# Kernel optimization log

Hardware: AMD Instinct MI355X
Metric: run time of the kernel (lower is better)

Reference implementation:

```python
import jax, jax.numpy as jnp
import numpy as np

D_MODEL = 1024
NUM_HEADS = 16
HEAD_DIM = D_MODEL // NUM_HEADS


def setup_inputs() -> dict:
    key = jax.random.key(0)
    k1, k2, k3, k4, k5 = jax.random.split(key, 5)
    scale = 1.0 / np.sqrt(D_MODEL)
    x = jax.random.normal(k1, (2, 2048, D_MODEL), dtype=jnp.float32)
    Wqkv = jax.random.uniform(k2, (D_MODEL, 3 * D_MODEL), jnp.float32, -scale, scale)
    bqkv = jax.random.uniform(k3, (3 * D_MODEL,), jnp.float32, -scale, scale)
    Wout = jax.random.uniform(k4, (D_MODEL, D_MODEL), jnp.float32, -scale, scale)
    bout = jax.random.uniform(k5, (D_MODEL,), jnp.float32, -scale, scale)
    return {"x": x, "Wqkv": Wqkv, "bqkv": bqkv, "Wout": Wout, "bout": bout}


def reference(x, Wqkv, bqkv, Wout, bout):
    B, S, _ = x.shape
    qkv = x @ Wqkv + bqkv                                   # [B, S, 3*D]
    # reshape to [B, S, H, 3*head_dim] then to [B, H, S, 3*head_dim]
    qkv = qkv.reshape(B, S, NUM_HEADS, 3 * HEAD_DIM).transpose(0, 2, 1, 3)
    q, k, v = jnp.split(qkv, 3, axis=-1)                    # each [B, H, S, hd]
    scaled = jnp.einsum("bhqd,bhkd->bhqk", q, k) / jnp.sqrt(jnp.float32(HEAD_DIM))
    attn = jax.nn.softmax(scaled, axis=-1)                  # [B, H, S, S]
    values = jnp.einsum("bhqk,bhkd->bhqd", attn, v)         # [B, H, S, hd]
    values = values.transpose(0, 2, 1, 3).reshape(B, S, D_MODEL)
    return values @ Wout + bout
```

## Files before the change

kernel.cpp:

```cpp
#include <hip/hip_runtime.h>


typedef __attribute__((ext_vector_type(8)))  short short8;
typedef __attribute__((ext_vector_type(4)))  short short4v;
typedef __attribute__((ext_vector_type(8)))  float float8;
typedef __attribute__((ext_vector_type(4)))  float f32x4;
typedef __attribute__((ext_vector_type(16))) float f32x16;
typedef __attribute__((ext_vector_type(4)))  int   int4v;

#define D_MODEL 1024
#define NHEAD   16
#define HD      64
#define SEQ     2048
#define N3      (3*D_MODEL)
#define MB      (1024*1024)

static __device__ __forceinline__ float bf2f(short s) {
    unsigned u = ((unsigned)(unsigned short)s) << 16;
    return __builtin_bit_cast(float, u);
}
static __device__ __forceinline__ short f2bf(float f) {
    unsigned u = __builtin_bit_cast(unsigned, f);
    u = (u + 0x7fff + ((u >> 16) & 1)) >> 16;
    return (short)u;
}
static __device__ __forceinline__ unsigned pkbf(float a, float b) {
    unsigned ua = __builtin_bit_cast(unsigned, a);
    ua = (ua + 0x7fff + ((ua >> 16) & 1)) >> 16;
    unsigned ub = __builtin_bit_cast(unsigned, b);
    ub = (ub + 0x7fff + ((ub >> 16) & 1)) & 0xffff0000u;
    return ua | ub;
}
static __device__ __forceinline__ void gl16(const short* g, short* l) {
    __builtin_amdgcn_global_load_lds(
        (const __attribute__((address_space(1))) unsigned int*)g,
        (__attribute__((address_space(3))) unsigned int*)l, 16, 0, 0);
}

__global__ __launch_bounds__(256) void prep(
    const float* __restrict__ x, const float* __restrict__ Wqkv,
    const float* __restrict__ Wout,
    short* __restrict__ Xh, short* __restrict__ Xl,
    short* __restrict__ Wh, short* __restrict__ Wl,
    short* __restrict__ Woh, short* __restrict__ Wol)
{
    __shared__ float tile[32][33];
    const int bid = blockIdx.x;
    const int tid = threadIdx.x;

    if (bid < 2048) {
        const int i = (bid * 256 + tid) * 8;
        const float8 v = *(const float8*)&x[i];
        short8 h, l;
#pragma unroll
        for (int j = 0; j < 8; ++j) {
            h[j] = f2bf(v[j]);
            l[j] = f2bf(v[j] - bf2f(h[j]));
        }
        *(short8*)&Xh[i] = h;
        *(short8*)&Xl[i] = l;
        return;
    }

    const float* in; short *hi, *lo; int K, N, bx, by;
    if (bid < 5120) {
        const int b2 = bid - 2048;
        in = Wqkv; hi = Wh; lo = Wl; K = D_MODEL; N = N3;
        bx = b2 % 96; by = b2 / 96;
    } else {
        const int b3 = bid - 5120;
        in = Wout; hi = Woh; lo = Wol; K = D_MODEL; N = D_MODEL;
        bx = b3 & 31; by = b3 >> 5;
    }
    const int n0 = bx * 32, k0 = by * 32;
    const int tx = tid & 31, ty = tid >> 5;
#pragma unroll
    for (int i = 0; i < 4; ++i)
        tile[ty + 8*i][tx] = in[(k0 + ty + 8*i) * N + (n0 + tx)];
    __syncthreads();
#pragma unroll
    for (int i = 0; i < 4; ++i) {
        const float v  = tile[tx][ty + 8*i];
        const short vh = f2bf(v);
        const short vl = f2bf(v - bf2f(vh));
        const int idx  = (n0 + ty + 8*i) * K + (k0 + tx);
        hi[idx] = vh;
        lo[idx] = vl;
    }
}

#define QBUF_SH 28672
#define OFF_AL  8192
#define OFF_BH  16384
#define OFF_BL  22528

__global__ __launch_bounds__(512, 2) void qkv_gemm8(
    const short* __restrict__ Xh, const short* __restrict__ Xl,
    const short* __restrict__ Bh, const short* __restrict__ Bl,
    const float* __restrict__ bias,
    short* __restrict__ Qo, short* __restrict__ Ko, short* __restrict__ Vt)
{
    __shared__ __attribute__((aligned(16))) short smem[2 * QBUF_SH];

    const int tid  = threadIdx.x;
    const int wave = tid >> 6, lane = tid & 63;
    const int q4 = lane >> 4, l16 = lane & 15;
    const int wr = wave >> 2, wc = wave & 3;

    const int flat = blockIdx.x;
    const int sw = (flat & 7) * 32 + (flat >> 3);
    const int mt = sw & 15, nt = sw >> 4;
    const int m0 = mt * 256, n0 = nt * 192;

    const short* srcp[7];
#pragma unroll
    for (int j = 0; j < 7; ++j) {
        const int id = j * 512 + tid;
        const short* s;
        if (id < 1024)      { s = &Xh[(size_t)(m0 + (id >> 2)) * D_MODEL + (id & 3) * 8]; }
        else if (id < 2048) { const int c = id - 1024; s = &Xl[(size_t)(m0 + (c >> 2)) * D_MODEL + (c & 3) * 8]; }
        else if (id < 2816) { const int c = id - 2048; s = &Bh[(size_t)(n0 + (c >> 2)) * D_MODEL + (c & 3) * 8]; }
        else                { const int c = id - 2816; s = &Bl[(size_t)(n0 + (c >> 2)) * D_MODEL + (c & 3) * 8]; }
        srcp[j] = s;
    }

    auto stage = [&](int b) {
#pragma unroll
        for (int j = 0; j < 7; ++j) {
            gl16(srcp[j], smem + b * QBUF_SH + (j * 512 + tid) * 8);
            srcp[j] += 32;
        }
    };

    f32x4 acc[8][3];
#pragma unroll
    for (int i = 0; i < 8; ++i)
#pragma unroll
        for (int j = 0; j < 3; ++j) acc[i][j] = (f32x4){0.f, 0.f, 0.f, 0.f};

    stage(0);
    asm volatile("s_waitcnt vmcnt(0)" ::: "memory");
    __builtin_amdgcn_s_barrier();

    for (int t = 0; t < 32; ++t) {
        const int cur = t & 1;
        const short* base = smem + cur * QBUF_SH;
        const short* Ah_s = base;
        const short* Al_s = base + OFF_AL;
        const short* Bh_s = base + OFF_BH;
        const short* Bl_s = base + OFF_BL;

        short8 bhf[3], blf[3];
#pragma unroll
        for (int p = 0; p < 4; ++p) {
            const int r0 = (wr * 128 + (2*p)   * 16 + l16) * 32 + q4 * 8;
            const int r1 = (wr * 128 + (2*p+1) * 16 + l16) * 32 + q4 * 8;
            const short8 a0h = *(const short8*)(Ah_s + r0);
            const short8 a0l = *(const short8*)(Al_s + r0);
            const short8 a1h = *(const short8*)(Ah_s + r1);
            const short8 a1l = *(const short8*)(Al_s + r1);
            if (p == 0) {
#pragma unroll
                for (int n = 0; n < 3; ++n) {
                    const int rb = (wc * 48 + n * 16 + l16) * 32 + q4 * 8;
                    bhf[n] = *(const short8*)(Bh_s + rb);
                    blf[n] = *(const short8*)(Bl_s + rb);
                }
                if (t < 31) stage(cur ^ 1);
            }
            __builtin_amdgcn_s_barrier();
            asm volatile("s_waitcnt lgkmcnt(0)" ::: "memory");
            __builtin_amdgcn_sched_barrier(0);
            __builtin_amdgcn_s_setprio(1);
#pragma unroll
            for (int n = 0; n < 3; ++n) {
                acc[2*p][n]   = __builtin_amdgcn_mfma_f32_16x16x32_bf16(a0h, bhf[n], acc[2*p][n],   0, 0, 0);
                acc[2*p][n]   = __builtin_amdgcn_mfma_f32_16x16x32_bf16(a0h, blf[n], acc[2*p][n],   0, 0, 0);
                acc[2*p][n]   = __builtin_amdgcn_mfma_f32_16x16x32_bf16(a0l, bhf[n], acc[2*p][n],   0, 0, 0);
                acc[2*p+1][n] = __builtin_amdgcn_mfma_f32_16x16x32_bf16(a1h, bhf[n], acc[2*p+1][n], 0, 0, 0);
                acc[2*p+1][n] = __builtin_amdgcn_mfma_f32_16x16x32_bf16(a1h, blf[n], acc[2*p+1][n], 0, 0, 0);
                acc[2*p+1][n] = __builtin_amdgcn_mfma_f32_16x16x32_bf16(a1l, bhf[n], acc[2*p+1][n], 0, 0, 0);
            }
            __builtin_amdgcn_s_setprio(0);
            if (p == 3) asm volatile("s_waitcnt vmcnt(0)" ::: "memory");
            __builtin_amdgcn_s_barrier();
        }
    }

    const float SCALE_Q = 0.125f * 1.4426950408889634f;
#pragma unroll
    for (int tj = 0; tj < 3; ++tj) {
        const int jj = wc * 48 + tj * 16 + l16;
        const int n  = nt * 192 + jj;
        const float bv = bias[n];
#pragma unroll
        for (int ti = 0; ti < 8; ++ti) {
            const int mb = m0 + wr * 128 + ti * 16 + q4 * 4;
            const int b = mb >> 11;
            const int s = mb & 2047;
            const int bh_ = b * NHEAD + nt;
            if (jj >= 128) {
                short4v v4;
#pragma unroll
                for (int r = 0; r < 4; ++r) v4[r] = f2bf(acc[ti][tj][r] + bv);
                *(short4v*)&Vt[(bh_ * HD + (jj - 128)) * SEQ + s] = v4;
            } else if (jj < 64) {
#pragma unroll
                for (int r = 0; r < 4; ++r)
                    Qo[(bh_ * SEQ + s + r) * HD + jj] = f2bf((acc[ti][tj][r] + bv) * SCALE_Q);
            } else {
#pragma unroll
                for (int r = 0; r < 4; ++r)
                    Ko[(bh_ * SEQ + s + r) * HD + (jj - 64)] = f2bf(acc[ti][tj][r] + bv);
            }
        }
    }
}

__global__ __launch_bounds__(256, 4) void attn_tscore(
    const short* __restrict__ Q, const short* __restrict__ K,
    const short* __restrict__ Vt,
    short* __restrict__ Ch, short* __restrict__ Cl)
{
    __shared__ __attribute__((aligned(16))) char smem[34816];
    short (*Ks)[72] = (short(*)[72])smem;
    short (*Vs)[40] = (short(*)[40])(smem + 4608);

    const int bh = blockIdx.x;
    const int qb = blockIdx.y;
    const int bi = bh >> 4, hi_ = bh & 15;

    const short* Qp  = Q  + bh * SEQ * HD;
    const short* Kp  = K  + bh * SEQ * HD;
    const short* Vtp = Vt + bh * HD * SEQ;

    const int tid  = threadIdx.x;
    const int wave = tid >> 6, lane = tid & 63;
    const int l5 = lane & 31, hf = lane >> 5;
    const int q0w = qb * 128 + wave * 32;

    short8 qf[4];
#pragma unroll
    for (int c = 0; c < 4; ++c)
        qf[c] = *(const short8*)&Qp[(q0w + l5) * HD + c * 16 + hf * 8];

    f32x16 oacc0 = (f32x16)(0.f), oacc1 = (f32x16)(0.f);
    float m = -1.0e30f, l = 0.f;

    const int sKr = tid >> 3, sKc = (tid & 7) * 8;
    const int sVr = tid >> 2, sVc = (tid & 3) * 8;

    for (int kc = 0; kc < 64; ++kc) {
        const int kbase = kc * 32;
        __syncthreads();
        *(short8*)&Ks[sKr][sKc] = *(const short8*)&Kp[(kbase + sKr) * HD + sKc];
        *(short8*)&Vs[sVr][sVc] = *(const short8*)&Vtp[sVr * SEQ + kbase + sVc];
        __syncthreads();

        f32x16 sacc = (f32x16)(0.f);
#pragma unroll
        for (int c = 0; c < 4; ++c) {
            const short8 ka = *(const short8*)&Ks[l5][c * 16 + hf * 8];
            sacc = __builtin_amdgcn_mfma_f32_32x32x16_bf16(ka, qf[c], sacc, 0, 0, 0);
        }

        float a0 = fmaxf(sacc[0], sacc[8]),  a1 = fmaxf(sacc[1], sacc[9]);
        float a2 = fmaxf(sacc[2], sacc[10]), a3 = fmaxf(sacc[3], sacc[11]);
        float a4 = fmaxf(sacc[4], sacc[12]), a5 = fmaxf(sacc[5], sacc[13]);
        float a6 = fmaxf(sacc[6], sacc[14]), a7 = fmaxf(sacc[7], sacc[15]);
        a0 = fmaxf(a0, a4); a1 = fmaxf(a1, a5); a2 = fmaxf(a2, a6); a3 = fmaxf(a3, a7);
        a0 = fmaxf(fmaxf(a0, a1), fmaxf(a2, a3));
        a0 = fmaxf(a0, __shfl_xor(a0, 32, 64));
        const float mnew  = fmaxf(m, a0);
        const float alpha = exp2f(m - mnew);

        float p[16];
#pragma unroll
        for (int i = 0; i < 16; ++i) p[i] = exp2f(sacc[i] - mnew);

        float s0 = p[0]+p[8], s1 = p[1]+p[9], s2 = p[2]+p[10], s3 = p[3]+p[11];
        float s4 = p[4]+p[12], s5 = p[5]+p[13], s6 = p[6]+p[14], s7 = p[7]+p[15];
        s0 += s4; s1 += s5; s2 += s6; s3 += s7;
        float rs = (s0 + s1) + (s2 + s3);
        rs += __shfl_xor(rs, 32, 64);
        l = l * alpha + rs;
        m = mnew;

#pragma unroll
        for (int i = 0; i < 16; ++i) { oacc0[i] *= alpha; oacc1[i] *= alpha; }

        unsigned u0 = pkbf(p[0],  p[1]),  u1 = pkbf(p[2],  p[3]);
        unsigned u2 = pkbf(p[4],  p[5]),  u3 = pkbf(p[6],  p[7]);
        unsigned u4 = pkbf(p[8],  p[9]),  u5 = pkbf(p[10], p[11]);
        unsigned u6 = pkbf(p[12], p[13]), u7 = pkbf(p[14], p[15]);
        const unsigned x0 = __shfl_xor(u0, 32, 64), x1 = __shfl_xor(u1, 32, 64);
        const unsigned x2 = __shfl_xor(u2, 32, 64), x3 = __shfl_xor(u3, 32, 64);
        const unsigned x4 = __shfl_xor(u4, 32, 64), x5 = __shfl_xor(u5, 32, 64);
        const unsigned x6 = __shfl_xor(u6, 32, 64), x7 = __shfl_xor(u7, 32, 64);
        int4v pb0 = (int4v){ (int)(hf ? x2 : u0), (int)(hf ? x3 : u1),
                             (int)(hf ? u2 : x0), (int)(hf ? u3 : x1) };
        int4v pb1 = (int4v){ (int)(hf ? x6 : u4), (int)(hf ? x7 : u5),
                             (int)(hf ? u6 : x4), (int)(hf ? u7 : x5) };
        const short8 pbf0 = __builtin_bit_cast(short8, pb0);
        const short8 pbf1 = __builtin_bit_cast(short8, pb1);

        {
            const short8 va00 = *(const short8*)&Vs[l5][hf * 8];
            const short8 va01 = *(const short8*)&Vs[l5][16 + hf * 8];
            oacc0 = __builtin_amdgcn_mfma_f32_32x32x16_bf16(va00, pbf0, oacc0, 0, 0, 0);
            oacc0 = __builtin_amdgcn_mfma_f32_32x32x16_bf16(va01, pbf1, oacc0, 0, 0, 0);
            const short8 va10 = *(const short8*)&Vs[32 + l5][hf * 8];
            const short8 va11 = *(const short8*)&Vs[32 + l5][16 + hf * 8];
            oacc1 = __builtin_amdgcn_mfma_f32_32x32x16_bf16(va10, pbf0, oacc1, 0, 0, 0);
            oacc1 = __builtin_amdgcn_mfma_f32_32x32x16_bf16(va11, pbf1, oacc1, 0, 0, 0);
        }
    }

    const float inv = 1.0f / l;
#pragma unroll
    for (int i = 0; i < 16; ++i) { oacc0[i] *= inv; oacc1[i] *= inv; }

    __syncthreads();
    float (*epi)[68] = (float(*)[68])(smem + wave * 8704);
#pragma unroll
    for (int r = 0; r < 16; ++r) {
        const int d = (r & 3) + 8 * (r >> 2) + 4 * hf;
        epi[l5][d]      = oacc0[r];
        epi[l5][32 + d] = oacc1[r];
    }
    __builtin_amdgcn_s_waitcnt(0);
#pragma unroll
    for (int pass = 0; pass < 8; ++pass) {
        const int row = pass * 4 + (lane >> 4);
        const int col = (lane & 15) * 4;
        const float4 v = *(const float4*)&epi[row][col];
        const float o[4] = {v.x, v.y, v.z, v.w};
        short4v hh, ll;
#pragma unroll
        for (int i = 0; i < 4; ++i) {
            hh[i] = f2bf(o[i]);
            ll[i] = f2bf(o[i] - bf2f(hh[i]));
        }
        const size_t co = ((size_t)(bi * SEQ + q0w + row)) * D_MODEL + hi_ * HD + col;
        *(short4v*)&Ch[co] = hh;
        *(short4v*)&Cl[co] = ll;
    }
}

__global__ __launch_bounds__(256) void out_gemm128(
    const short* __restrict__ Ah, const short* __restrict__ Al,
    const short* __restrict__ Bh, const short* __restrict__ Bl,
    const float* __restrict__ bias, float* __restrict__ out)
{
    __shared__ short AhS[128*32], AlS[128*32], BhS[128*32], BlS[128*32];

    const int tid  = threadIdx.x;
    const int wave = tid >> 6, lane = tid & 63;
    const int q4 = lane >> 4, l16 = lane & 15;
    const int m0 = blockIdx.y * 128, n0 = blockIdx.x * 128;
    const int rw = (wave & 1) * 64, cw = (wave >> 1) * 64;
    const int trow = tid >> 2;
    const int tcol = (tid & 3) * 8;

    f32x4 acc[4][4];
#pragma unroll
    for (int i = 0; i < 4; ++i)
#pragma unroll
        for (int j = 0; j < 4; ++j) acc[i][j] = (f32x4){0.f, 0.f, 0.f, 0.f};

    for (int kt = 0; kt < D_MODEL; kt += 32) {
        gl16(&Ah[(m0 + trow) * D_MODEL + kt + tcol],      AhS + tid * 8);
        gl16(&Ah[(m0 + 64 + trow) * D_MODEL + kt + tcol], AhS + 2048 + tid * 8);
        gl16(&Al[(m0 + trow) * D_MODEL + kt + tcol],      AlS + tid * 8);
        gl16(&Al[(m0 + 64 + trow) * D_MODEL + kt + tcol], AlS + 2048 + tid * 8);
        gl16(&Bh[(n0 + trow) * D_MODEL + kt + tcol],      BhS + tid * 8);
        gl16(&Bh[(n0 + 64 + trow) * D_MODEL + kt + tcol], BhS + 2048 + tid * 8);
        gl16(&Bl[(n0 + trow) * D_MODEL + kt + tcol],      BlS + tid * 8);
        gl16(&Bl[(n0 + 64 + trow) * D_MODEL + kt + tcol], BlS + 2048 + tid * 8);
        __syncthreads();

        short8 ah[4], al[4], bh[4], bl[4];
#pragma unroll
        for (int t = 0; t < 4; ++t) {
            ah[t] = *(const short8*)&AhS[(rw + t * 16 + l16) * 32 + q4 * 8];
            al[t] = *(const short8*)&AlS[(rw + t * 16 + l16) * 32 + q4 * 8];
            bh[t] = *(const short8*)&BhS[(cw + t * 16 + l16) * 32 + q4 * 8];
            bl[t] = *(const short8*)&BlS[(cw + t * 16 + l16) * 32 + q4 * 8];
        }
#pragma unroll
        for (int ti = 0; ti < 4; ++ti)
#pragma unroll
            for (int tj = 0; tj < 4; ++tj) {
                acc[ti][tj] = __builtin_amdgcn_mfma_f32_16x16x32_bf16(ah[ti], bh[tj], acc[ti][tj], 0, 0, 0);
                acc[ti][tj] = __builtin_amdgcn_mfma_f32_16x16x32_bf16(ah[ti], bl[tj], acc[ti][tj], 0, 0, 0);
                acc[ti][tj] = __builtin_amdgcn_mfma_f32_16x16x32_bf16(al[ti], bh[tj], acc[ti][tj], 0, 0, 0);
            }
        __syncthreads();
    }

#pragma unroll
    for (int tj = 0; tj < 4; ++tj) {
        const int n = n0 + cw + tj * 16 + l16;
        const float bv = bias[n];
#pragma unroll
        for (int ti = 0; ti < 4; ++ti) {
            const int mb = m0 + rw + ti * 16 + q4 * 4;
#pragma unroll
            for (int r = 0; r < 4; ++r)
                out[(mb + r) * D_MODEL + n] = acc[ti][tj][r] + bv;
        }
    }
}

extern "C" void kernel_launch(void* const* d_in, const int* in_sizes, int n_in,
                              void* d_out, int out_size, void* d_ws, size_t ws_size,
                              hipStream_t stream)
{
    const float* x    = (const float*)d_in[0];
    const float* Wqkv = (const float*)d_in[1];
    const float* bqkv = (const float*)d_in[2];
    const float* Wout = (const float*)d_in[3];
    const float* bout = (const float*)d_in[4];
    float* out = (float*)d_out;

    char* ws = (char*)d_ws;
    short* Qb  = (short*)(ws);
    short* Kb  = (short*)(ws +  8*MB);
    short* Vtb = (short*)(ws + 16*MB);
    short* Woh = (short*)(ws + 24*MB);
    short* Wol = (short*)(ws + 26*MB);
    short* Ch  = (short*)(ws + 28*MB);
    short* Cl  = (short*)(ws + 36*MB);
    short* Xh  = (short*)(ws + 44*MB);
    short* Xl  = (short*)(ws + 52*MB);
    short* Wh  = (short*)(ws + 60*MB);
    short* Wl  = (short*)(ws + 66*MB);

    prep<<<6144, 256, 0, stream>>>(x, Wqkv, Wout, Xh, Xl, Wh, Wl, Woh, Wol);
    qkv_gemm8<<<dim3(256), 512, 0, stream>>>(Xh, Xl, Wh, Wl, bqkv, Qb, Kb, Vtb);
    attn_tscore<<<dim3(32, 16), 256, 0, stream>>>(Qb, Kb, Vtb, Ch, Cl);
    out_gemm128<<<dim3(8, 32), 256, 0, stream>>>(Ch, Cl, Woh, Wol, bout, out);
}
```

Measured before the change: 295.7 us.

## Double-buffer K/V tiles with 64-key chunks and lazy softmax rescaling in attention

The attention kernel now processes 64 keys per iteration instead of 32, using two LDS buffers. The next chunk is prefetched into registers while the current one is computed, so only one barrier is needed per iteration. The running max is updated only when the new max exceeds the old by more than 8 (log2 domain), which skips most rescales of the accumulators. bf16 packing now uses the hardware v_cvt_pk_bf16_f32 instruction. Launch bounds drop to 2 blocks per SM to allow more registers, which may reduce occupancy.

```diff
diff --git a/kernel.cpp b/kernel.cpp
--- a/kernel.cpp
+++ b/kernel.cpp
@@ -30,6 +30,11 @@
     unsigned ub = __builtin_bit_cast(unsigned, b);
     ub = (ub + 0x7fff + ((ub >> 16) & 1)) & 0xffff0000u;
     return ua | ub;
+}
+static __device__ __forceinline__ unsigned cvtpk(float a, float b) {
+    unsigned r;
+    asm("v_cvt_pk_bf16_f32 %0, %1, %2" : "=v"(r) : "v"(a), "v"(b));
+    return r;
 }
 static __device__ __forceinline__ void gl16(const short* g, short* l) {
     __builtin_amdgcn_global_load_lds(
@@ -217,14 +222,14 @@
     }
 }
 
-__global__ __launch_bounds__(256, 4) void attn_tscore(
+__global__ __launch_bounds__(256, 2) void attn_tscore(
     const short* __restrict__ Q, const short* __restrict__ K,
     const short* __restrict__ Vt,
     short* __restrict__ Ch, short* __restrict__ Cl)
 {
-    __shared__ __attribute__((aligned(16))) char smem[34816];
+    __shared__ __attribute__((aligned(16))) char smem[36864];
     short (*Ks)[72] = (short(*)[72])smem;
-    short (*Vs)[40] = (short(*)[40])(smem + 4608);
+    short (*Vs)[72] = (short(*)[72])(smem + 18432);
 
     const int bh = blockIdx.x;
     const int qb = blockIdx.y;
@@ -247,80 +252,133 @@
     f32x16 oacc0 = (f32x16)(0.f), oacc1 = (f32x16)(0.f);
     float m = -1.0e30f, l = 0.f;
 
-    const int sKr = tid >> 3, sKc = (tid & 7) * 8;
-    const int sVr = tid >> 2, sVc = (tid & 3) * 8;
-
-    for (int kc = 0; kc < 64; ++kc) {
-        const int kbase = kc * 32;
-        __syncthreads();
-        *(short8*)&Ks[sKr][sKc] = *(const short8*)&Kp[(kbase + sKr) * HD + sKc];
-        *(short8*)&Vs[sVr][sVc] = *(const short8*)&Vtp[sVr * SEQ + kbase + sVc];
-        __syncthreads();
-
-        f32x16 sacc = (f32x16)(0.f);
+    const int sr = tid >> 2;
+    const int sc = (tid & 3) * 16;
+
+    short8 kr0 = *(const short8*)&Kp[sr * HD + sc];
+    short8 kr1 = *(const short8*)&Kp[sr * HD + sc + 8];
+    short8 vr0 = *(const short8*)&Vtp[sr * SEQ + sc];
+    short8 vr1 = *(const short8*)&Vtp[sr * SEQ + sc + 8];
+    *(short8*)&Ks[sr][sc]     = kr0;
+    *(short8*)&Ks[sr][sc + 8] = kr1;
+    *(short8*)&Vs[sr][sc]     = vr0;
+    *(short8*)&Vs[sr][sc + 8] = vr1;
+    __syncthreads();
+
+    for (int kc = 0; kc < 32; ++kc) {
+        const int buf = (kc & 1) << 6;
+
+        if (kc < 31) {
+            const int nkb = (kc + 1) << 6;
+            kr0 = *(const short8*)&Kp[(nkb + sr) * HD + sc];
+            kr1 = *(const short8*)&Kp[(nkb + sr) * HD + sc + 8];
+            vr0 = *(const short8*)&Vtp[sr * SEQ + nkb + sc];
+            vr1 = *(const short8*)&Vtp[sr * SEQ + nkb + sc + 8];
+        }
+
+        f32x16 s0 = (f32x16)(0.f), s1 = (f32x16)(0.f);
 #pragma unroll
         for (int c = 0; c < 4; ++c) {
-            const short8 ka = *(const short8*)&Ks[l5][c * 16 + hf * 8];
-            sacc = __builtin_amdgcn_mfma_f32_32x32x16_bf16(ka, qf[c], sacc, 0, 0, 0);
-        }
-
-        float a0 = fmaxf(sacc[0], sacc[8]),  a1 = fmaxf(sacc[1], sacc[9]);
-        float a2 = fmaxf(sacc[2], sacc[10]), a3 = fmaxf(sacc[3], sacc[11]);
-        float a4 = fmaxf(sacc[4], sacc[12]), a5 = fmaxf(sacc[5], sacc[13]);
-        float a6 = fmaxf(sacc[6], sacc[14]), a7 = fmaxf(sacc[7], sacc[15]);
-        a0 = fmaxf(a0, a4); a1 = fmaxf(a1, a5); a2 = fmaxf(a2, a6); a3 = fmaxf(a3, a7);
-        a0 = fmaxf(fmaxf(a0, a1), fmaxf(a2, a3));
-        a0 = fmaxf(a0, __shfl_xor(a0, 32, 64));
-        const float mnew  = fmaxf(m, a0);
-        const float alpha = exp2f(m - mnew);
-
-        float p[16];
-#pragma unroll
-        for (int i = 0; i < 16; ++i) p[i] = exp2f(sacc[i] - mnew);
-
-        float s0 = p[0]+p[8], s1 = p[1]+p[9], s2 = p[2]+p[10], s3 = p[3]+p[11];
-        float s4 = p[4]+p[12], s5 = p[5]+p[13], s6 = p[6]+p[14], s7 = p[7]+p[15];
-        s0 += s4; s1 += s5; s2 += s6; s3 += s7;
-        float rs = (s0 + s1) + (s2 + s3);
+            const short8 ka0 = *(const short8*)&Ks[buf + l5][c * 16 + hf * 8];
+            const short8 ka1 = *(const short8*)&Ks[buf + 32 + l5][c * 16 + hf * 8];
+            s0 = __builtin_amdgcn_mfma_f32_32x32x16_bf16(ka0, qf[c], s0, 0, 0, 0);
+            s1 = __builtin_amdgcn_mfma_f32_32x32x16_bf16(ka1, qf[c], s1, 0, 0, 0);
+        }
+
+        float t[8];
+#pragma unroll
+        for (int i = 0; i < 8; ++i)
+            t[i] = fmaxf(fmaxf(s0[i], s0[i + 8]), fmaxf(s1[i], s1[i + 8]));
+        float pmax = fmaxf(fmaxf(fmaxf(t[0], t[1]), fmaxf(t[2], t[3])),
+                           fmaxf(fmaxf(t[4], t[5]), fmaxf(t[6], t[7])));
+        pmax = fmaxf(pmax, __shfl_xor(pmax, 32, 64));
+
+        if (!__all(pmax - m <= 8.0f)) {
+            const float mnew  = fmaxf(m, pmax);
+            const float alpha = exp2f(m - mnew);
+#pragma unroll
+            for (int i = 0; i < 16; ++i) { oacc0[i] *= alpha; oacc1[i] *= alpha; }
+            l *= alpha;
+            m = mnew;
+        }
+
+        float p0[16], p1[16];
+#pragma unroll
+        for (int i = 0; i < 16; ++i) { p0[i] = exp2f(s0[i] - m); p1[i] = exp2f(s1[i] - m); }
+        float sa = 0.f, sb = 0.f, sc_ = 0.f, sd = 0.f;
+#pragma unroll
+        for (int i = 0; i < 4; ++i) {
+            sa += p0[i] + p0[i + 8];
+            sb += p0[i + 4] + p0[i + 12];
+            sc_ += p1[i] + p1[i + 8];
+            sd += p1[i + 4] + p1[i + 12];
+        }
+        float rs = (sa + sb) + (sc_ + sd);
         rs += __shfl_xor(rs, 32, 64);
-        l = l * alpha + rs;
-        m = mnew;
-
-#pragma unroll
-        for (int i = 0; i < 16; ++i) { oacc0[i] *= alpha; oacc1[i] *= alpha; }
-
-        unsigned u0 = pkbf(p[0],  p[1]),  u1 = pkbf(p[2],  p[3]);
-        unsigned u2 = pkbf(p[4],  p[5]),  u3 = pkbf(p[6],  p[7]);
-        unsigned u4 = pkbf(p[8],  p[9]),  u5 = pkbf(p[10], p[11]);
-        unsigned u6 = pkbf(p[12], p[13]), u7 = pkbf(p[14], p[15]);
+        l += rs;
+
+        unsigned u0 = cvtpk(p0[0],  p0[1]),  u1 = cvtpk(p0[2],  p0[3]);
+        unsigned u2 = cvtpk(p0[4],  p0[5]),  u3 = cvtpk(p0[6],  p0[7]);
+        unsigned u4 = cvtpk(p0[8],  p0[9]),  u5 = cvtpk(p0[10], p0[11]);
+        unsigned u6 = cvtpk(p0[12], p0[13]), u7 = cvtpk(p0[14], p0[15]);
+        unsigned w0 = cvtpk(p1[0],  p1[1]),  w1 = cvtpk(p1[2],  p1[3]);
+        unsigned w2 = cvtpk(p1[4],  p1[5]),  w3 = cvtpk(p1[6],  p1[7]);
+        unsigned w4 = cvtpk(p1[8],  p1[9]),  w5 = cvtpk(p1[10], p1[11]);
+        unsigned w6 = cvtpk(p1[12], p1[13]), w7 = cvtpk(p1[14], p1[15]);
         const unsigned x0 = __shfl_xor(u0, 32, 64), x1 = __shfl_xor(u1, 32, 64);
         const unsigned x2 = __shfl_xor(u2, 32, 64), x3 = __shfl_xor(u3, 32, 64);
         const unsigned x4 = __shfl_xor(u4, 32, 64), x5 = __shfl_xor(u5, 32, 64);
         const unsigned x6 = __shfl_xor(u6, 32, 64), x7 = __shfl_xor(u7, 32, 64);
+        const unsigned y0 = __shfl_xor(w0, 32, 64), y1 = __shfl_xor(w1, 32, 64);
+        const unsigned y2 = __shfl_xor(w2, 32, 64), y3 = __shfl_xor(w3, 32, 64);
+        const unsigned y4 = __shfl_xor(w4, 32, 64), y5 = __shfl_xor(w5, 32, 64);
+        const unsigned y6 = __shfl_xor(w6, 32, 64), y7 = __shfl_xor(w7, 32, 64);
         int4v pb0 = (int4v){ (int)(hf ? x2 : u0), (int)(hf ? x3 : u1),
                              (int)(hf ? u2 : x0), (int)(hf ? u3 : x1) };
         int4v pb1 = (int4v){ (int)(hf ? x6 : u4), (int)(hf ? x7 : u5),
                              (int)(hf ? u6 : x4), (int)(hf ? u7 : x5) };
+        int4v pb2 = (int4v){ (int)(hf ? y2 : w0), (int)(hf ? y3 : w1),
+                             (int)(hf ? w2 : y0), (int)(hf ? w3 : y1) };
+        int4v pb3 = (int4v){ (int)(hf ? y6 : w4), (int)(hf ? y7 : w5),
+                             (int)(hf ? w6 : y4), (int)(hf ? w7 : y5) };
         const short8 pbf0 = __builtin_bit_cast(short8, pb0);
         const short8 pbf1 = __builtin_bit_cast(short8, pb1);
+        const short8 pbf2 = __builtin_bit_cast(short8, pb2);
+        const short8 pbf3 = __builtin_bit_cast(short8, pb3);
 
         {
-            const short8 va00 = *(const short8*)&Vs[l5][hf * 8];
-            const short8 va01 = *(const short8*)&Vs[l5][16 + hf * 8];
-            oacc0 = __builtin_amdgcn_mfma_f32_32x32x16_bf16(va00, pbf0, oacc0, 0, 0, 0);
-            oacc0 = __builtin_amdgcn_mfma_f32_32x32x16_bf16(va01, pbf1, oacc0, 0, 0, 0);
-            const short8 va10 = *(const short8*)&Vs[32 + l5][hf * 8];
-            const short8 va11 = *(const short8*)&Vs[32 + l5][16 + hf * 8];
-            oacc1 = __builtin_amdgcn_mfma_f32_32x32x16_bf16(va10, pbf0, oacc1, 0, 0, 0);
-            oacc1 = __builtin_amdgcn_mfma_f32_32x32x16_bf16(va11, pbf1, oacc1, 0, 0, 0);
-        }
+            const short8 va0 = *(const short8*)&Vs[buf + l5][hf * 8];
+            const short8 va1 = *(const short8*)&Vs[buf + l5][16 + hf * 8];
+            const short8 va2 = *(const short8*)&Vs[buf + l5][32 + hf * 8];
+            const short8 va3 = *(const short8*)&Vs[buf + l5][48 + hf * 8];
+            oacc0 = __builtin_amdgcn_mfma_f32_32x32x16_bf16(va0, pbf0, oacc0, 0, 0, 0);
+            oacc0 = __builtin_amdgcn_mfma_f32_32x32x16_bf16(va1, pbf1, oacc0, 0, 0, 0);
+            oacc0 = __builtin_amdgcn_mfma_f32_32x32x16_bf16(va2, pbf2, oacc0, 0, 0, 0);
+            oacc0 = __builtin_amdgcn_mfma_f32_32x32x16_bf16(va3, pbf3, oacc0, 0, 0, 0);
+            const short8 vb0 = *(const short8*)&Vs[buf + 32 + l5][hf * 8];
+            const short8 vb1 = *(const short8*)&Vs[buf + 32 + l5][16 + hf * 8];
+            const short8 vb2 = *(const short8*)&Vs[buf + 32 + l5][32 + hf * 8];
+            const short8 vb3 = *(const short8*)&Vs[buf + 32 + l5][48 + hf * 8];
+            oacc1 = __builtin_amdgcn_mfma_f32_32x32x16_bf16(vb0, pbf0, oacc1, 0, 0, 0);
+            oacc1 = __builtin_amdgcn_mfma_f32_32x32x16_bf16(vb1, pbf1, oacc1, 0, 0, 0);
+            oacc1 = __builtin_amdgcn_mfma_f32_32x32x16_bf16(vb2, pbf2, oacc1, 0, 0, 0);
+            oacc1 = __builtin_amdgcn_mfma_f32_32x32x16_bf16(vb3, pbf3, oacc1, 0, 0, 0);
+        }
+
+        if (kc < 31) {
+            const int wb = ((kc + 1) & 1) << 6;
+            *(short8*)&Ks[wb + sr][sc]     = kr0;
+            *(short8*)&Ks[wb + sr][sc + 8] = kr1;
+            *(short8*)&Vs[wb + sr][sc]     = vr0;
+            *(short8*)&Vs[wb + sr][sc + 8] = vr1;
+        }
+        __syncthreads();
     }
 
     const float inv = 1.0f / l;
 #pragma unroll
     for (int i = 0; i < 16; ++i) { oacc0[i] *= inv; oacc1[i] *= inv; }
 
-    __syncthreads();
     float (*epi)[68] = (float(*)[68])(smem + wave * 8704);
 #pragma unroll
     for (int r = 0; r < 16; ++r) {
```

After: 280.1 us. 5.3% less time.
